# Performance work log

Hardware: AMD Instinct MI355X
Metric: run time of the kernel (lower is better)

## Reference

```python
import jax, jax.numpy as jnp
import numpy as np

N_HEAD = 4
IN_FEAT = 512
N_FEAT = 512
D_K = N_FEAT // N_HEAD
KERNEL = 11
SANM_SHIFT = 0
LEFT_PAD = (KERNEL - 1) // 2 + SANM_SHIFT
RIGHT_PAD = KERNEL - 1 - LEFT_PAD
B, T = 16, 1024
NEG = -1e9  # stand-in for -inf (grad-safe)


def setup_inputs() -> dict:
    key = jax.random.key(0)
    ks = jax.random.split(key, 6)
    x = jax.random.normal(ks[0], (B, T, IN_FEAT), dtype=jnp.float32)
    # padding mask: first 3/4 of frames valid, tail padded (as in batched ASR)
    valid = (jnp.arange(T) < (3 * T) // 4).astype(jnp.float32)
    mask = jnp.broadcast_to(valid[None, None, :], (B, 1, T))
    s = 1.0 / np.sqrt(IN_FEAT)
    w_qkv = jax.random.uniform(ks[1], (IN_FEAT, 3 * N_FEAT), jnp.float32, -s, s)
    b_qkv = jnp.zeros((3 * N_FEAT,), jnp.float32)
    so = 1.0 / np.sqrt(N_FEAT)
    w_out = jax.random.uniform(ks[2], (N_FEAT, N_FEAT), jnp.float32, -so, so)
    b_out = jnp.zeros((N_FEAT,), jnp.float32)
    # depthwise Conv1d weight: (channels, k)
    w_fsmn = jax.random.uniform(ks[3], (N_FEAT, KERNEL), jnp.float32, -1.0 / np.sqrt(KERNEL), 1.0 / np.sqrt(KERNEL))
    return {"x": x, "mask": mask, "w_qkv": w_qkv, "b_qkv": b_qkv,
            "w_out": w_out, "b_out": b_out, "w_fsmn": w_fsmn}


def _fsmn(v, mask_bt1, w_fsmn):
    # v: (B,T,D); mask_bt1: (B,T,1)
    inp = v * mask_bt1
    xc = jnp.transpose(inp, (0, 2, 1))                      # (B,D,T)
    xc = jnp.pad(xc, ((0, 0), (0, 0), (LEFT_PAD, RIGHT_PAD)))
    y = jax.lax.conv_general_dilated(
        xc, w_fsmn[:, None, :], window_strides=(1,), padding='VALID',
        feature_group_count=N_FEAT, dimension_numbers=('NCH', 'OIH', 'NCH'))
    y = jnp.transpose(y, (0, 2, 1)) + inp                   # residual
    return y * mask_bt1                                     # re-zero padded frames


def _forward(x, mask, w_qkv, b_qkv, w_out, b_out, w_fsmn):
    b, t, _ = x.shape
    qkv = x @ w_qkv + b_qkv                                 # (B,T,3D)
    q, k, v = jnp.split(qkv, 3, axis=-1)
    qh = q.reshape(b, t, N_HEAD, D_K).transpose(0, 2, 1, 3) # (B,H,T,dk)
    kh = k.reshape(b, t, N_HEAD, D_K).transpose(0, 2, 1, 3)
    vh = v.reshape(b, t, N_HEAD, D_K).transpose(0, 2, 1, 3)

    fsmn_mem = _fsmn(v, mask.reshape(b, t, 1), w_fsmn)

    scale = D_K ** (-0.5)
    scores = jnp.einsum('bhqd,bhkd->bhqk', qh * scale, kh)  # (B,H,T,T)
    m0 = (mask[:, None, :, :] == 0)                         # (B,1,1,T)
    scores = jnp.where(m0, NEG, scores)
    attn = jax.nn.softmax(scores, axis=-1)
    attn = jnp.where(m0, 0.0, attn)
    ctx = jnp.einsum('bhqk,bhkd->bhqd', attn, vh)
    ctx = ctx.transpose(0, 2, 1, 3).reshape(b, t, N_FEAT)
    att_out = ctx @ w_out + b_out
    return att_out + fsmn_mem


def reference(x, mask, w_qkv, b_qkv, w_out, b_out, w_fsmn):
    return _forward(x, mask, w_qkv, b_qkv, w_out, b_out, w_fsmn)
```

## Files before the change

kernel.cpp:

```cpp
#include <hip/hip_runtime.h>
#include <stdint.h>

#define SCALE_Q 0.08838834764831845f
#define LOG2E 1.4426950408889634f
#define NEGBIG -1e30f

typedef __attribute__((ext_vector_type(4))) float f32x4;
typedef __attribute__((ext_vector_type(16))) float f32x16;
typedef __attribute__((ext_vector_type(8))) short s16x8;
typedef __attribute__((ext_vector_type(4))) unsigned u32x4;

static __device__ __forceinline__ unsigned short f2bf(float f) {
  unsigned int u = __builtin_bit_cast(unsigned int, f);
  u += 0x7FFFu + ((u >> 16) & 1u);
  return (unsigned short)(u >> 16);
}
static __device__ __forceinline__ float bf2f(unsigned short b) {
  unsigned int u = ((unsigned int)b) << 16;
  return __builtin_bit_cast(float, u);
}

static __device__ __forceinline__ unsigned cvt_pk_bf16(float lo, float hi) {
  unsigned r;
  asm("v_cvt_pk_bf16_f32 %0, %1, %2" : "=v"(r) : "v"(lo), "v"(hi));
  return r;
}

static __device__ __forceinline__ float xchg_max(float x) {
  float a = x, b = x;
  asm("v_permlane32_swap_b32 %0, %1" : "+v"(a), "+v"(b));
  return fmaxf(a, b);
}
static __device__ __forceinline__ float xchg_sum(float x) {
  float a = x, b = x;
  asm("v_permlane32_swap_b32 %0, %1" : "+v"(a), "+v"(b));
  return a + b;
}

static __device__ __forceinline__ float vmax16(const f32x16& v) {
  float a = fmaxf(fmaxf(fmaxf(v[0], v[1]), fmaxf(v[2], v[3])),
                  fmaxf(fmaxf(v[4], v[5]), fmaxf(v[6], v[7])));
  float b = fmaxf(fmaxf(fmaxf(v[8], v[9]), fmaxf(v[10], v[11])),
                  fmaxf(fmaxf(v[12], v[13]), fmaxf(v[14], v[15])));
  return fmaxf(a, b);
}

static __device__ __forceinline__ void gload16(const void* g, void* l) {
  __builtin_amdgcn_global_load_lds(
      (const __attribute__((address_space(1))) void*)g,
      (__attribute__((address_space(3))) void*)l, 16, 0, 0);
}

__global__ void k_convert_x(const float* __restrict__ x, unsigned short* __restrict__ xb) {
  int i = (blockIdx.x * 256 + threadIdx.x) * 8;
  const float4* p = reinterpret_cast<const float4*>(x + i);
  float4 a = p[0], b = p[1];
  s16x8 o;
  o[0] = f2bf(a.x); o[1] = f2bf(a.y); o[2] = f2bf(a.z); o[3] = f2bf(a.w);
  o[4] = f2bf(b.x); o[5] = f2bf(b.y); o[6] = f2bf(b.z); o[7] = f2bf(b.w);
  *reinterpret_cast<s16x8*>(xb + i) = o;
}

__global__ void k_transpose_bf(const float* __restrict__ w, unsigned short* __restrict__ wt, int Nd) {
  int gid = blockIdx.x * 256 + threadIdx.x;
  int n = gid >> 6;
  int k0 = (gid & 63) * 8;
  if (n >= Nd) return;
  s16x8 o;
#pragma unroll
  for (int j = 0; j < 8; ++j) o[j] = f2bf(w[(size_t)(k0 + j) * Nd + n]);
  *reinterpret_cast<s16x8*>(wt + (size_t)n * 512 + k0) = o;
}

template <int MODE>
__launch_bounds__(256, 2)
__global__ void k_gemm(const unsigned short* __restrict__ A,
                       const unsigned short* __restrict__ Bt,
                       const float* __restrict__ bias,
                       const float* __restrict__ mask,
                       const float* __restrict__ wf,
                       const unsigned short* __restrict__ vsrc,
                       unsigned short* __restrict__ qs, unsigned short* __restrict__ kbuf,
                       unsigned short* __restrict__ vbf, unsigned short* __restrict__ vt,
                       float* __restrict__ outp,
                       int tiles_n, int cpx) {
  __shared__ unsigned short smem[32768];
  int bid0 = blockIdx.x;
  int bid = (bid0 & 7) * cpx + (bid0 >> 3);
  int rb = bid / tiles_n, cb = bid % tiles_n;
  int tid = threadIdx.x;
  int w = tid >> 6, lane = tid & 63;
  int g = lane >> 4, ln = lane & 15;
  int wr = w >> 1, wc = w & 1;

  if constexpr (MODE == 0) {
    if (cb >= 4) {
      int b = (rb * 128) >> 10, t0 = (rb * 128) & 1023;
      const float* mb = mask + b * 1024 + t0;
      float a0 = mb[lane * 2], a1 = mb[lane * 2 + 1];
      if (__ballot(a0 != 0.f || a1 != 0.f) == 0ull) return;
    }
  }

  int sr = lane >> 3;
  int sc = lane & 7;

  auto stage = [&](int kb0, int bsel) {
    unsigned short* al = smem + bsel * 16384;
    unsigned short* bl = al + 8192;
#pragma unroll
    for (int it = 0; it < 4; ++it) {
      int r0 = it * 32 + w * 8;
      int r = r0 + sr;
      int cg = sc ^ (r & 7);
      gload16(A + (size_t)(rb * 128 + r) * 512 + kb0 + cg * 8, al + r0 * 64);
      gload16(Bt + (size_t)(cb * 128 + r) * 512 + kb0 + cg * 8, bl + r0 * 64);
    }
  };

  f32x4 acc[4][4] = {};

  stage(0, 0);
  __syncthreads();
  int cur = 0;
  for (int kt = 0; kt < 8; ++kt) {
    if (kt < 7) stage((kt + 1) * 64, cur ^ 1);
    const unsigned short* al = smem + cur * 16384;
    const unsigned short* bl = al + 8192;
#pragma unroll
    for (int kk = 0; kk < 2; ++kk) {
      s16x8 af[4], bf[4];
#pragma unroll
      for (int m = 0; m < 4; ++m) {
        int row = wr * 64 + m * 16 + ln;
        af[m] = *reinterpret_cast<const s16x8*>(al + row * 64 + (((kk * 4 + g) ^ (row & 7)) * 8));
      }
#pragma unroll
      for (int n = 0; n < 4; ++n) {
        int row = wc * 64 + n * 16 + ln;
        bf[n] = *reinterpret_cast<const s16x8*>(bl + row * 64 + (((kk * 4 + g) ^ (row & 7)) * 8));
      }
#pragma unroll
      for (int m = 0; m < 4; ++m)
#pragma unroll
        for (int n = 0; n < 4; ++n)
          acc[m][n] = __builtin_amdgcn_mfma_f32_16x16x32_bf16(af[m], bf[n], acc[m][n], 0, 0, 0);
    }
    __syncthreads();
    cur ^= 1;
  }

  int c0 = cb * 128;
  int R0 = rb * 128 + wr * 64;

  if constexpr (MODE == 0) {
#pragma unroll
    for (int m = 0; m < 4; ++m) {
#pragma unroll
      for (int n = 0; n < 4; ++n) {
        int col = c0 + wc * 64 + n * 16 + ln;
        int Rbase = R0 + m * 16 + g * 4;
        float bv = bias[col];
        int which = col >> 9;
        int h = (col >> 7) & 3;
        int d = col & 127;
        int b = Rbase >> 10, t0 = Rbase & 1023;
        if (which == 2) {
          unsigned short pk[4];
#pragma unroll
          for (int r = 0; r < 4; ++r) {
            float v = acc[m][n][r] + bv;
            pk[r] = f2bf(v);
            vbf[(size_t)(Rbase + r) * 512 + (col - 1024)] = pk[r];
          }
          uint2 uv;
          uv.x = (unsigned)pk[0] | ((unsigned)pk[1] << 16);
          uv.y = (unsigned)pk[2] | ((unsigned)pk[3] << 16);
          *reinterpret_cast<uint2*>(vt + ((size_t)((b * 4 + h) * 128 + d)) * 1024 + t0) = uv;
        } else {
          unsigned short* dst = (which == 0) ? qs : kbuf;
          float sc2 = (which == 0) ? (SCALE_Q * LOG2E) : 1.0f;
#pragma unroll
          for (int r = 0; r < 4; ++r) {
            int t = t0 + r;
            dst[((size_t)((b * 4 + h) * 1024 + t)) * 128 + d] = f2bf((acc[m][n][r] + bv) * sc2);
          }
        }
      }
    }
  } else {
    int b = (rb * 128) >> 10, tloc0 = (rb * 128) & 1023;
    unsigned short* vh = smem;
    float* wl = reinterpret_cast<float*>(smem + 18816);
    for (int idx = tid; idx < 138 * 16; idx += 256) {
      int i = idx >> 4, gc = idx & 15;
      int tl = tloc0 - 5 + i;
      s16x8 v8 = {};
      if (tl >= 0 && tl < 1024) {
        if (mask[b * 1024 + tl] != 0.f)
          v8 = *reinterpret_cast<const s16x8*>(vsrc + ((size_t)b * 1024 + tl) * 512 + c0 + gc * 8);
      }
      *reinterpret_cast<s16x8*>(vh + i * 136 + gc * 8) = v8;
    }
    if (tid < 128) {
#pragma unroll
      for (int j = 0; j < 11; ++j) wl[tid * 11 + j] = wf[(c0 + tid) * 11 + j];
    }
    __syncthreads();

#pragma unroll
    for (int m = 0; m < 4; ++m) {
      int Rbase = R0 + m * 16 + g * 4;
      int lrb = Rbase - rb * 128;
      float mk[4];
#pragma unroll
      for (int r = 0; r < 4; ++r) mk[r] = mask[b * 1024 + ((Rbase + r) & 1023)];
#pragma unroll
      for (int n = 0; n < 4; ++n) {
        int lc = wc * 64 + n * 16 + ln;
        int col = c0 + lc;
        float bv = bias[col];
        float win[14];
#pragma unroll
        for (int i = 0; i < 14; ++i) win[i] = bf2f(vh[(lrb + i) * 136 + lc]);
        float wj[11];
#pragma unroll
        for (int j = 0; j < 11; ++j) wj[j] = wl[lc * 11 + j];
#pragma unroll
        for (int r = 0; r < 4; ++r) {
          float conv = win[r + 5];
#pragma unroll
          for (int j = 0; j < 11; ++j) conv += wj[j] * win[r + j];
          size_t idx = (size_t)(Rbase + r) * 512 + col;
          outp[idx] = acc[m][n][r] + bv + conv * mk[r];
        }
      }
    }
  }
}

__launch_bounds__(512, 1)
__global__ void k_attn(const unsigned short* __restrict__ qs,
                       const unsigned short* __restrict__ kbuf,
                       const unsigned short* __restrict__ vt,
                       const float* __restrict__ mask,
                       unsigned short* __restrict__ ctx) {
  __shared__ unsigned short smem[2 * 32768];

  int bid0 = blockIdx.x;
  int bid = (bid0 & 7) * 32 + (bid0 >> 3);
  int qc = bid & 3;
  int bh = bid >> 2;
  int b = bh >> 2, h = bh & 3;
  int tid = threadIdx.x;
  int w = tid >> 6, l = tid & 63;
  int half = l >> 5, lq = l & 31;

  const unsigned short* kbase = kbuf + (size_t)bh * 1024 * 128;
  const unsigned short* vtbase = vt + (size_t)bh * 128 * 1024;
  const float* mbase = mask + b * 1024;

  s16x8 aq[8];
  {
    const unsigned short* qrow = qs + ((size_t)bh * 1024 + qc * 256 + w * 32 + lq) * 128 + half * 8;
#pragma unroll
    for (int c = 0; c < 8; ++c)
      aq[c] = *reinterpret_cast<const s16x8*>(qrow + c * 16);
  }

  s16x8 bone = {};
  bone[0] = (short)(half == 0 ? 0x3F80 : 0);

  f32x16 o[4] = {};
  float M = NEGBIG, L = 0.f;

  unsigned amask = 0;
  for (int kb = 0; kb < 8; ++kb) {
    float m0 = mbase[kb * 128 + l];
    float m1 = mbase[kb * 128 + 64 + l];
    if (__ballot((m0 != 0.f) || (m1 != 0.f)) != 0ull) amask |= (1u << kb);
  }

  auto stage = [&](int kb, int bsel) {
    unsigned short* kd = smem + bsel * 32768;
    unsigned short* vd = kd + 16384;
    int srl = l >> 4;
    int scl = l & 15;
#pragma unroll
    for (int it = 0; it < 4; ++it) {
      int r0 = it * 32 + w * 4;
      int r = r0 + srl;
      int cg = scl ^ (r & 15);
      gload16(kbase + (size_t)(kb * 128 + r) * 128 + cg * 8, kd + r0 * 128);
      gload16(vtbase + (size_t)r * 1024 + kb * 128 + cg * 8, vd + r0 * 128);
    }
  };

  unsigned rem = amask;
  int kb_cur = __ffs(rem) - 1; rem &= rem - 1;
  stage(kb_cur, 0);
  __syncthreads();
  int cur = 0;

  while (true) {
    int kb_next = rem ? (__ffs(rem) - 1) : -1;
    if (kb_next >= 0) { rem &= rem - 1; stage(kb_next, cur ^ 1); }

    unsigned short* kl = smem + cur * 32768;
    unsigned short* vl = kl + 16384;

    f32x16 s[4];
    __builtin_amdgcn_s_setprio(1);
#pragma unroll
    for (int kt = 0; kt < 4; ++kt) {
      float mv = mbase[kb_cur * 128 + kt * 32 + lq];
      s16x8 ba = {};
      ba[0] = (short)((half == 0 && mv == 0.f) ? (short)0xFF7F : 0);
      f32x16 z = {};
      s[kt] = __builtin_amdgcn_mfma_f32_32x32x16_bf16(ba, bone, z, 0, 0, 0);
      int row = kt * 32 + lq, rx = row & 15;
#pragma unroll
      for (int c = 0; c < 8; ++c) {
        s16x8 kf = *reinterpret_cast<const s16x8*>(kl + row * 128 + (((c * 2 + half) ^ rx) * 8));
        s[kt] = __builtin_amdgcn_mfma_f32_32x32x16_bf16(kf, aq[c], s[kt], 0, 0, 0);
      }
    }
    __builtin_amdgcn_s_setprio(0);

    float mx = fmaxf(fmaxf(vmax16(s[0]), vmax16(s[1])), fmaxf(vmax16(s[2]), vmax16(s[3])));
    mx = xchg_max(mx);
    float mnew = fmaxf(M, mx);
    float alpha = exp2f(M - mnew);
    M = mnew;
    float ls0 = 0.f, ls1 = 0.f, ls2 = 0.f, ls3 = 0.f;
#pragma unroll
    for (int kt = 0; kt < 4; ++kt) {
#pragma unroll
      for (int i = 0; i < 16; ++i) {
        float p = exp2f(s[kt][i] - M);
        s[kt][i] = p;
        if ((i & 3) == 0) ls0 += p; else if ((i & 3) == 1) ls1 += p;
        else if ((i & 3) == 2) ls2 += p; else ls3 += p;
      }
    }
    float ls = (ls0 + ls1) + (ls2 + ls3);
    ls = xchg_sum(ls);
    L = L * alpha + ls;
#pragma unroll
    for (int dt = 0; dt < 4; ++dt)
#pragma unroll
      for (int i = 0; i < 16; ++i) o[dt][i] *= alpha;

    __builtin_amdgcn_s_setprio(1);
#pragma unroll
    for (int kt = 0; kt < 4; ++kt) {
      unsigned w0 = cvt_pk_bf16(s[kt][0], s[kt][1]);
      unsigned w1 = cvt_pk_bf16(s[kt][2], s[kt][3]);
      unsigned w2 = cvt_pk_bf16(s[kt][4], s[kt][5]);
      unsigned w3 = cvt_pk_bf16(s[kt][6], s[kt][7]);
      unsigned w4 = cvt_pk_bf16(s[kt][8], s[kt][9]);
      unsigned w5 = cvt_pk_bf16(s[kt][10], s[kt][11]);
      unsigned w6 = cvt_pk_bf16(s[kt][12], s[kt][13]);
      unsigned w7 = cvt_pk_bf16(s[kt][14], s[kt][15]);
      asm("v_permlane32_swap_b32 %0, %1" : "+v"(w0), "+v"(w2));
      asm("v_permlane32_swap_b32 %0, %1" : "+v"(w1), "+v"(w3));
      asm("v_permlane32_swap_b32 %0, %1" : "+v"(w4), "+v"(w6));
      asm("v_permlane32_swap_b32 %0, %1" : "+v"(w5), "+v"(w7));
      u32x4 f0 = {w0, w1, w2, w3};
      u32x4 f1 = {w4, w5, w6, w7};
      s16x8 p0 = __builtin_bit_cast(s16x8, f0);
      s16x8 p1 = __builtin_bit_cast(s16x8, f1);
#pragma unroll
      for (int dt = 0; dt < 4; ++dt) {
        int row = dt * 32 + lq, rx = row & 15;
        s16x8 va = *reinterpret_cast<const s16x8*>(vl + row * 128 + (((kt * 4 + half) ^ rx) * 8));
        o[dt] = __builtin_amdgcn_mfma_f32_32x32x16_bf16(va, p0, o[dt], 0, 0, 0);
        s16x8 vb = *reinterpret_cast<const s16x8*>(vl + row * 128 + (((kt * 4 + 2 + half) ^ rx) * 8));
        o[dt] = __builtin_amdgcn_mfma_f32_32x32x16_bf16(vb, p1, o[dt], 0, 0, 0);
      }
    }
    __builtin_amdgcn_s_setprio(0);

    if (kb_next < 0) break;
    __syncthreads();
    kb_cur = kb_next; cur ^= 1;
  }

  float inv = 1.0f / L;
  __syncthreads();
  unsigned short* obuf = smem;
#pragma unroll
  for (int dt = 0; dt < 4; ++dt) {
#pragma unroll
    for (int g = 0; g < 4; ++g) {
      int d0 = dt * 32 + g * 8 + half * 4;
      unsigned lo = cvt_pk_bf16(o[dt][g * 4 + 0] * inv, o[dt][g * 4 + 1] * inv);
      unsigned hi = cvt_pk_bf16(o[dt][g * 4 + 2] * inv, o[dt][g * 4 + 3] * inv);
      int row = w * 32 + lq;
      int gr = d0 >> 2;
      uint2 uv; uv.x = lo; uv.y = hi;
      *reinterpret_cast<uint2*>(obuf + row * 128 + ((gr ^ (row & 15)) * 4)) = uv;
    }
  }
  __syncthreads();
  size_t cbase = ((size_t)b * 1024 + qc * 256) * 512 + h * 128;
#pragma unroll
  for (int it = 0; it < 16; ++it) {
    int chunk = it * 512 + tid;
    int row = chunk >> 5, gr = chunk & 31;
    uint2 v = *reinterpret_cast<uint2*>(obuf + row * 128 + ((gr ^ (row & 15)) * 4));
    *reinterpret_cast<uint2*>(ctx + cbase + (size_t)row * 512 + gr * 4) = v;
  }
}

extern "C" void kernel_launch(void* const* d_in, const int* in_sizes, int n_in,
                              void* d_out, int out_size, void* d_ws, size_t ws_size,
                              hipStream_t stream) {
  const float* x      = (const float*)d_in[0];
  const float* mask   = (const float*)d_in[1];
  const float* w_qkv  = (const float*)d_in[2];
  const float* b_qkv  = (const float*)d_in[3];
  const float* w_out  = (const float*)d_in[4];
  const float* b_out  = (const float*)d_in[5];
  const float* w_fsmn = (const float*)d_in[6];
  float* out = (float*)d_out;

  char* ws = (char*)d_ws;
  size_t off = 0;
  auto alloc = [&](size_t bytes) { void* p = ws + off; off += (bytes + 255) & ~(size_t)255; return p; };
  unsigned short* x_bf   = (unsigned short*)alloc(16384ull * 512 * 2);
  unsigned short* wT_qkv = (unsigned short*)alloc(1536ull * 512 * 2);
  unsigned short* wT_out = (unsigned short*)alloc(512ull * 512 * 2);
  unsigned short* qs     = (unsigned short*)alloc(64ull * 1024 * 128 * 2);
  unsigned short* kbuf   = (unsigned short*)alloc(64ull * 1024 * 128 * 2);
  unsigned short* vt     = (unsigned short*)alloc(64ull * 128 * 1024 * 2);
  unsigned short* vbf    = (unsigned short*)alloc(16384ull * 512 * 2);
  unsigned short* ctx    = (unsigned short*)alloc(16384ull * 512 * 2);

  k_convert_x<<<4096, 256, 0, stream>>>(x, x_bf);
  k_transpose_bf<<<(1536 * 64) / 256, 256, 0, stream>>>(w_qkv, wT_qkv, 1536);
  k_transpose_bf<<<(512 * 64) / 256, 256, 0, stream>>>(w_out, wT_out, 512);
  k_gemm<0><<<128 * 12, 256, 0, stream>>>(x_bf, wT_qkv, b_qkv, mask, nullptr, nullptr,
                                          qs, kbuf, vbf, vt, nullptr, 12, (128 * 12) / 8);
  k_attn<<<256, 512, 0, stream>>>(qs, kbuf, vt, mask, ctx);
  k_gemm<1><<<128 * 4, 256, 0, stream>>>(ctx, wT_out, b_out, mask, w_fsmn, vbf,
                                         nullptr, nullptr, nullptr, nullptr, out, 4, (128 * 4) / 8);
}
```

Before: 205.0 us.

## Merge prep kernels, add lazy softmax rescale, reshape max reduction

Three small prep kernels (x conversion and two weight transposes) are merged into one launch to cut launch overhead. In the attention inner loop, the running max and the rescale of O and L are now updated only when some lane's new block max exceeds the stored max by more than 8 (log2 domain). Otherwise rescaling is skipped, saving 64 multiplies and an exp per iteration at the cost of a wave-wide vote and unnormalized exponents up to 2^8. The max16 reduction is also regrouped into 3-input max chains, presumably to map onto v_max3.

```diff
diff --git a/kernel.cpp b/kernel.cpp
--- a/kernel.cpp
+++ b/kernel.cpp
@@ -38,11 +38,13 @@
 }
 
 static __device__ __forceinline__ float vmax16(const f32x16& v) {
-  float a = fmaxf(fmaxf(fmaxf(v[0], v[1]), fmaxf(v[2], v[3])),
-                  fmaxf(fmaxf(v[4], v[5]), fmaxf(v[6], v[7])));
-  float b = fmaxf(fmaxf(fmaxf(v[8], v[9]), fmaxf(v[10], v[11])),
-                  fmaxf(fmaxf(v[12], v[13]), fmaxf(v[14], v[15])));
-  return fmaxf(a, b);
+  float m0 = fmaxf(fmaxf(v[0], v[1]), v[2]);
+  float m1 = fmaxf(fmaxf(v[3], v[4]), v[5]);
+  float m2 = fmaxf(fmaxf(v[6], v[7]), v[8]);
+  float m3 = fmaxf(fmaxf(v[9], v[10]), v[11]);
+  float m4 = fmaxf(fmaxf(v[12], v[13]), v[14]);
+  float m5 = fmaxf(fmaxf(v[15], m0), m1);
+  return fmaxf(fmaxf(fmaxf(m2, m3), m4), m5);
 }
 
 static __device__ __forceinline__ void gload16(const void* g, void* l) {
@@ -51,25 +53,34 @@
       (__attribute__((address_space(3))) void*)l, 16, 0, 0);
 }
 
-__global__ void k_convert_x(const float* __restrict__ x, unsigned short* __restrict__ xb) {
-  int i = (blockIdx.x * 256 + threadIdx.x) * 8;
-  const float4* p = reinterpret_cast<const float4*>(x + i);
-  float4 a = p[0], b = p[1];
-  s16x8 o;
-  o[0] = f2bf(a.x); o[1] = f2bf(a.y); o[2] = f2bf(a.z); o[3] = f2bf(a.w);
-  o[4] = f2bf(b.x); o[5] = f2bf(b.y); o[6] = f2bf(b.z); o[7] = f2bf(b.w);
-  *reinterpret_cast<s16x8*>(xb + i) = o;
-}
-
-__global__ void k_transpose_bf(const float* __restrict__ w, unsigned short* __restrict__ wt, int Nd) {
-  int gid = blockIdx.x * 256 + threadIdx.x;
-  int n = gid >> 6;
-  int k0 = (gid & 63) * 8;
-  if (n >= Nd) return;
-  s16x8 o;
-#pragma unroll
-  for (int j = 0; j < 8; ++j) o[j] = f2bf(w[(size_t)(k0 + j) * Nd + n]);
-  *reinterpret_cast<s16x8*>(wt + (size_t)n * 512 + k0) = o;
+__global__ void k_prep(const float* __restrict__ x, unsigned short* __restrict__ xb,
+                       const float* __restrict__ w_qkv, unsigned short* __restrict__ wtq,
+                       const float* __restrict__ w_out, unsigned short* __restrict__ wto) {
+  int bid = blockIdx.x;
+  int tid = threadIdx.x;
+  if (bid < 4096) {
+    int i = (bid * 256 + tid) * 8;
+    const float4* p = reinterpret_cast<const float4*>(x + i);
+    float4 a = p[0], b = p[1];
+    s16x8 o;
+    o[0] = f2bf(a.x); o[1] = f2bf(a.y); o[2] = f2bf(a.z); o[3] = f2bf(a.w);
+    o[4] = f2bf(b.x); o[5] = f2bf(b.y); o[6] = f2bf(b.z); o[7] = f2bf(b.w);
+    *reinterpret_cast<s16x8*>(xb + i) = o;
+  } else if (bid < 4096 + 384) {
+    int gid = (bid - 4096) * 256 + tid;
+    int n = gid >> 6, k0 = (gid & 63) * 8;
+    s16x8 o;
+#pragma unroll
+    for (int j = 0; j < 8; ++j) o[j] = f2bf(w_qkv[(size_t)(k0 + j) * 1536 + n]);
+    *reinterpret_cast<s16x8*>(wtq + (size_t)n * 512 + k0) = o;
+  } else {
+    int gid = (bid - 4480) * 256 + tid;
+    int n = gid >> 6, k0 = (gid & 63) * 8;
+    s16x8 o;
+#pragma unroll
+    for (int j = 0; j < 8; ++j) o[j] = f2bf(w_out[(size_t)(k0 + j) * 512 + n]);
+    *reinterpret_cast<s16x8*>(wto + (size_t)n * 512 + k0) = o;
+  }
 }
 
 template <int MODE>
@@ -329,9 +340,16 @@
 
     float mx = fmaxf(fmaxf(vmax16(s[0]), vmax16(s[1])), fmaxf(vmax16(s[2]), vmax16(s[3])));
     mx = xchg_max(mx);
-    float mnew = fmaxf(M, mx);
-    float alpha = exp2f(M - mnew);
-    M = mnew;
+    if (!__all(mx <= M + 8.f)) {
+      float mnew = fmaxf(M, mx);
+      float alpha = exp2f(M - mnew);
+      M = mnew;
+      L *= alpha;
+#pragma unroll
+      for (int dt = 0; dt < 4; ++dt)
+#pragma unroll
+        for (int i = 0; i < 16; ++i) o[dt][i] *= alpha;
+    }
     float ls0 = 0.f, ls1 = 0.f, ls2 = 0.f, ls3 = 0.f;
 #pragma unroll
     for (int kt = 0; kt < 4; ++kt) {
@@ -345,11 +363,7 @@
     }
     float ls = (ls0 + ls1) + (ls2 + ls3);
     ls = xchg_sum(ls);
-    L = L * alpha + ls;
-#pragma unroll
-    for (int dt = 0; dt < 4; ++dt)
-#pragma unroll
-      for (int i = 0; i < 16; ++i) o[dt][i] *= alpha;
+    L += ls;
 
     __builtin_amdgcn_s_setprio(1);
 #pragma unroll
@@ -437,9 +451,7 @@
   unsigned short* vbf    = (unsigned short*)alloc(16384ull * 512 * 2);
   unsigned short* ctx    = (unsigned short*)alloc(16384ull * 512 * 2);
 
-  k_convert_x<<<4096, 256, 0, stream>>>(x, x_bf);
-  k_transpose_bf<<<(1536 * 64) / 256, 256, 0, stream>>>(w_qkv, wT_qkv, 1536);
-  k_transpose_bf<<<(512 * 64) / 256, 256, 0, stream>>>(w_out, wT_out, 512);
+  k_prep<<<4608, 256, 0, stream>>>(x, x_bf, w_qkv, wT_qkv, w_out, wT_out);
   k_gemm<0><<<128 * 12, 256, 0, stream>>>(x_bf, wT_qkv, b_qkv, mask, nullptr, nullptr,
                                           qs, kbuf, vbf, vt, nullptr, 12, (128 * 12) / 8);
   k_attn<<<256, 512, 0, stream>>>(qs, kbuf, vt, mask, ctx);
```

After: 201.1 us. No clear change (-1.9%).
